# Kernel tuning notes

Measured on AMD Instinct MI355X. Metric: run time of the kernel, lower is better.

The kernel has to match this reference:

```python
import jax, jax.numpy as jnp
import numpy as np

B, Q, G = 32, 16384, 128   # batch, num queries, (padded) num GT per image
K = 32                      # first top-k (nearest candidates per GT)
N = 9                       # second top-k (highest-IoU matches per GT)


def box_cxcywh_to_xyxy(b):
    cx, cy, w, h = jnp.split(b, 4, axis=-1)
    return jnp.concatenate([cx - 0.5 * w, cy - 0.5 * h,
                            cx + 0.5 * w, cy + 0.5 * h], axis=-1)


def box_iou(a, b):
    # a, b: broadcastable [..., 4] in xyxy
    lt = jnp.maximum(a[..., :2], b[..., :2])
    rb = jnp.minimum(a[..., 2:], b[..., 2:])
    wh = jnp.clip(rb - lt, 0.0)
    inter = wh[..., 0] * wh[..., 1]
    area_a = (a[..., 2] - a[..., 0]) * (a[..., 3] - a[..., 1])
    area_b = (b[..., 2] - b[..., 0]) * (b[..., 3] - b[..., 1])
    return inter / (area_a + area_b - inter)


def _assign(gt, pred):
    # gt: [G,4] cxcywh, pred: [Q,4] cxcywh
    # euclidean cdist in cxcywh space: [G, Q]
    d = jnp.sqrt(jnp.sum((gt[:, None, :] - pred[None, :, :]) ** 2, axis=-1))
    # k nearest predictions per GT (smallest distance)
    _, kidx = jax.lax.top_k(-d, K)            # [G, K]
    k_boxes = pred[kidx]                       # [G, K, 4]
    iou = box_iou(box_cxcywh_to_xyxy(gt)[:, None, :],
                  box_cxcywh_to_xyxy(k_boxes))           # [G, K]
    vals, ns = jax.lax.top_k(iou, N)           # [G, N] highest IoU among the K
    pred_idx = jnp.take_along_axis(kidx, ns, axis=1)      # [G, N] global pred ids
    gt_idx = jnp.broadcast_to(jnp.arange(gt.shape[0])[:, None], ns.shape)
    return pred_idx.reshape(-1), gt_idx.reshape(-1)


def setup_inputs() -> dict:
    key = jax.random.key(0)
    k1, k2 = jax.random.split(key)
    pred_boxes = jax.random.uniform(k1, (B, Q, 4), dtype=jnp.float32)
    gt_boxes = jax.random.uniform(k2, (B, G, 4), dtype=jnp.float32)
    return {"pred_boxes": pred_boxes, "gt_boxes": gt_boxes}


def reference(pred_boxes, gt_boxes):
    # per-image assignment, vectorized over the batch
    pred_idx, gt_idx = jax.vmap(_assign)(gt_boxes, pred_boxes)
    # pred_idx, gt_idx: [B, G*N] int32 (analog of the list of (i, j) index tensors)
    return pred_idx, gt_idx
```

## Files before the change

### kernel.cpp

```cpp
#include <hip/hip_runtime.h>

#define BB 32
#define QQ 16384
#define GG 128
#define KK 32
#define NN 9
#define TT 16
#define TH 1024
#define RR (QQ / TH)
#define NW (TH / 64)
#define CAP 192
#define ACAP 96
#define UF 4

typedef unsigned long long u64;
typedef unsigned int u32;

#define INFF __uint_as_float(0x7F800000u)

__device__ __forceinline__ u64 pack_asc(float key, u32 idx) {
  return (((u64)__float_as_uint(key)) << 32) | (u64)idx;
}

__device__ __forceinline__ float dist2_ref(const float4 g, const float4 p) {
#pragma clang fp contract(off)
  float dx = g.x - p.x;
  float dy = g.y - p.y;
  float dz = g.z - p.z;
  float dw = g.w - p.w;
  float s = dx * dx + dy * dy;
  s = s + dz * dz;
  s = s + dw * dw;
  return s;
}

__device__ __forceinline__ float iou_ref(const float4 g, const float4 p) {
#pragma clang fp contract(off)
  float gx1 = g.x - 0.5f * g.z, gy1 = g.y - 0.5f * g.w;
  float gx2 = g.x + 0.5f * g.z, gy2 = g.y + 0.5f * g.w;
  float px1 = p.x - 0.5f * p.z, py1 = p.y - 0.5f * p.w;
  float px2 = p.x + 0.5f * p.z, py2 = p.y + 0.5f * p.w;
  float ltx = fmaxf(gx1, px1), lty = fmaxf(gy1, py1);
  float rbx = fminf(gx2, px2), rby = fminf(gy2, py2);
  float wx = fmaxf(rbx - ltx, 0.0f), wy = fmaxf(rby - lty, 0.0f);
  float inter = wx * wy;
  float aa = (gx2 - gx1) * (gy2 - gy1);
  float ab = (px2 - px1) * (py2 - py1);
  return inter / ((aa + ab) - inter);
}

__device__ __forceinline__ u64 bitonic64(u64 v, int lane) {
#pragma unroll
  for (int k = 2; k <= 64; k <<= 1) {
#pragma unroll
    for (int j = k >> 1; j > 0; j >>= 1) {
      u64 o = __shfl_xor(v, j, 64);
      bool up = ((lane & k) == 0);
      bool lower = ((lane & j) == 0);
      v = (lower == up) ? (v < o ? v : o) : (v > o ? v : o);
    }
  }
  return v;
}

__device__ __forceinline__ u64 bitonic32(u64 v, int lane) {
#pragma unroll
  for (int k = 2; k <= 32; k <<= 1) {
#pragma unroll
    for (int j = k >> 1; j > 0; j >>= 1) {
      u64 o = __shfl_xor(v, j, 64);
      bool up = ((lane & k) == 0);
      bool lower = ((lane & j) == 0);
      v = (lower == up) ? (v < o ? v : o) : (v > o ? v : o);
    }
  }
  return v;
}

__device__ __forceinline__ u32 f2ord(float f) {
  u32 b = __float_as_uint(f);
  return (b & 0x80000000u) ? ~b : (b | 0x80000000u);
}
__device__ __forceinline__ float ord2f(u32 k) {
  return __uint_as_float((k & 0x80000000u) ? (k & 0x7FFFFFFFu) : ~k);
}

__global__ __launch_bounds__(TH, 4) void atss_kernel(
    const float4* __restrict__ pred, const float4* __restrict__ gtb,
    int* __restrict__ out) {
  __shared__ float smin[TT][TH];
  __shared__ float ckey[TT][CAP];
  __shared__ unsigned short cidx[TT][CAP];
  __shared__ unsigned short sact[TT][ACAP];
  __shared__ int kidx[TT][KK];
  __shared__ int nC[TT];
  __shared__ int nAct[TT];

  const int t = threadIdx.x;
  const int f = blockIdx.x;
  const int b = (f & 7) * 4 + (f >> 6);
  const int g0 = ((f >> 3) & 7) * TT;

  if (t < TT) {
    nC[t] = 0;
    nAct[t] = 0;
  }

  float4 G[TT];
#pragma unroll
  for (int gg = 0; gg < TT; ++gg) G[gg] = gtb[b * GG + g0 + gg];

  const float4* pb = pred + (size_t)b * QQ;

  float mn[TT];
#pragma unroll
  for (int gg = 0; gg < TT; ++gg) mn[gg] = INFF;

  float4 P[UF];
#pragma unroll
  for (int u = 0; u < UF; ++u) P[u] = pb[t + u * TH];
#pragma unroll
  for (int j = 0; j < RR; j += UF) {
    float4 C[UF];
#pragma unroll
    for (int u = 0; u < UF; ++u) C[u] = P[u];
    if (j + UF < RR) {
#pragma unroll
      for (int u = 0; u < UF; ++u) P[u] = pb[t + (j + UF + u) * TH];
    }
#pragma unroll
    for (int u = 0; u < UF; ++u) {
      float4 p = C[u];
      float pp = fmaf(p.x, p.x, fmaf(p.y, p.y, fmaf(p.z, p.z, p.w * p.w)));
      float qx = p.x + p.x, qy = p.y + p.y, qz = p.z + p.z, qw = p.w + p.w;
#pragma unroll
      for (int gg = 0; gg < TT; ++gg) {
        float acc = fmaf(-G[gg].x, qx, pp);
        acc = fmaf(-G[gg].y, qy, acc);
        acc = fmaf(-G[gg].z, qz, acc);
        acc = fmaf(-G[gg].w, qw, acc);
        mn[gg] = fminf(mn[gg], acc);
      }
    }
  }
#pragma unroll
  for (int gg = 0; gg < TT; ++gg) smin[gg][t] = mn[gg];

  __syncthreads();

  const int w = t >> 6;
  const int lane = t & 63;

  const float4 gt = gtb[b * GG + g0 + w];

  float V[NW];
#pragma unroll
  for (int k = 0; k < NW; ++k) V[k] = smin[w][lane + 64 * k];

  float m1 = INFF, m2 = INFF;
#pragma unroll
  for (int k = 0; k < NW; ++k) {
    float v = V[k];
    float nm1 = fminf(m1, v);
    m2 = fminf(m2, fmaxf(m1, v));
    m1 = nm1;
  }

  u32 k1 = f2ord(m1), k2 = f2ord(m2);
  u32 pref = 0;
#pragma unroll
  for (int bit = 31; bit >= 0; --bit) {
    u32 tr = pref | (1u << bit);
    int c = __popcll(__ballot(k1 < tr)) + __popcll(__ballot(k2 < tr));
    if (c < 32) pref = tr;
  }
  float Us = ord2f(pref);

  float gg2 = fmaf(gt.x, gt.x,
              fmaf(gt.y, gt.y, fmaf(gt.z, gt.z, gt.w * gt.w)));
  const float sUs = Us + fabsf(Us) * 2e-5f + 4e-6f;
  const float T = fmaxf(Us + gg2, 0.0f) * 1.00002f + 4e-6f;

#pragma unroll
  for (int k = 0; k < NW; ++k) {
    if (V[k] <= sUs) {
      int pos = atomicAdd(&nAct[w], 1);
      if (pos < ACAP) sact[w][pos] = (unsigned short)(lane + 64 * k);
    }
  }
  int na = nAct[w];

  if (na <= ACAP) {
    int total = na * RR;
    int it = lane;
    int i0 = 0;
    float4 p0;
    if (it < total) {
      int r = sact[w][it >> 4];
      i0 = r + (it & 15) * TH;
      p0 = pb[i0];
    }
    while (it < total) {
      int itn = it + 64;
      int i1 = 0;
      float4 p1;
      if (itn < total) {
        int r = sact[w][itn >> 4];
        i1 = r + (itn & 15) * TH;
        p1 = pb[i1];
      }
      float d2 = dist2_ref(gt, p0);
      if (d2 <= T) {
        int pos = atomicAdd(&nC[w], 1);
        if (pos < CAP) {
          ckey[w][pos] = d2;
          cidx[w][pos] = (unsigned short)i0;
        }
      }
      it = itn;
      i0 = i1;
      p0 = p1;
    }
  } else {
    for (int r = lane; r < TH; r += 64) {
      for (int j = 0; j < RR; ++j) {
        int i = r + j * TH;
        float d2 = dist2_ref(gt, pb[i]);
        if (d2 <= T) {
          int pos = atomicAdd(&nC[w], 1);
          if (pos < CAP) {
            ckey[w][pos] = d2;
            cidx[w][pos] = (unsigned short)i;
          }
        }
      }
    }
  }
  int n = nC[w];

  if (n > CAP) {
    if (lane == 0) {
      u64 best[KK];
      for (int l = 0; l < KK; ++l) best[l] = ~0ull;
      for (int i = 0; i < QQ; ++i) {
        float d = sqrtf(dist2_ref(gt, pb[i]));
        u64 pk = pack_asc(d, (u32)i);
        if (pk < best[KK - 1]) {
          int pos = KK - 1;
          while (pos > 0 && best[pos - 1] > pk) {
            best[pos] = best[pos - 1];
            --pos;
          }
          best[pos] = pk;
        }
      }
      for (int l = 0; l < KK; ++l) kidx[w][l] = (int)(best[l] & 0xFFFFFFFFull);
    }
  } else if (n <= 64) {
    u64 v = (lane < n) ? pack_asc(sqrtf(ckey[w][lane]), (u32)cidx[w][lane])
                       : ~0ull;
    u64 s = bitonic64(v, lane);
    if (lane < KK) kidx[w][lane] = (int)(s & 0xFFFFFFFFull);
  } else {
    volatile float* vk = ckey[w];
    for (int sel = 0; sel < KK; ++sel) {
      u64 lm = ~0ull;
      int ls = -1;
      for (int s = lane; s < n; s += 64) {
        float d = sqrtf(vk[s]);
        u64 pk = pack_asc(d, (u32)cidx[w][s]);
        if (pk < lm) {
          lm = pk;
          ls = s;
        }
      }
      u64 ww = lm;
#pragma unroll
      for (int j = 32; j > 0; j >>= 1) {
        u64 o = __shfl_xor(ww, j, 64);
        ww = o < ww ? o : ww;
      }
      if (lm == ww && ls >= 0) {
        vk[ls] = INFF;
        kidx[w][sel] = (int)(ww & 0xFFFFFFFFull);
      }
    }
  }

  {
    u64 v = ~0ull;
    if (lane < KK) {
      float iou = iou_ref(gt, pb[kidx[w][lane]]);
      v = (((u64)(~__float_as_uint(iou))) << 32) | (u64)lane;
    }
    u64 s = bitonic32(v, lane);
    if (lane < NN) {
      int pos = (int)(s & 0xFFFFFFFFull);
      int base = (b * GG + g0 + w) * NN + lane;
      out[base] = kidx[w][pos];
      out[BB * GG * NN + base] = g0 + w;
    }
  }
}

extern "C" void kernel_launch(void* const* d_in, const int* in_sizes, int n_in,
                              void* d_out, int out_size, void* d_ws, size_t ws_size,
                              hipStream_t stream) {
  (void)in_sizes;
  (void)n_in;
  (void)out_size;
  (void)d_ws;
  (void)ws_size;
  const float4* pred = (const float4*)d_in[0];
  const float4* gt = (const float4*)d_in[1];
  int* out = (int*)d_out;
  atss_kernel<<<(GG / TT) * BB, TH, 0, stream>>>(pred, gt, out);
}
```

Baseline: 79.47 us.

## Replace shared atomics with ballot compaction and bitonic sorts with rank-based selection

Shared-memory atomic counters for active rows and candidates are replaced by wave-ballot prefix compaction, which removes the LDS atomics and the counter initialisation. The candidate gather loop is restructured with a 4-deep manual prefetch in place of 1-deep. The bitonic sorts for the top-32 distances and top-9 IoU are replaced by O(n) shuffle-based rank counting with ds_permute scatter, which trades log-depth compare-swap stages for a linear shuffle loop.

```diff
diff --git a/kernel.cpp b/kernel.cpp
--- a/kernel.cpp
+++ b/kernel.cpp
@@ -49,34 +49,6 @@
   return inter / ((aa + ab) - inter);
 }
 
-__device__ __forceinline__ u64 bitonic64(u64 v, int lane) {
-#pragma unroll
-  for (int k = 2; k <= 64; k <<= 1) {
-#pragma unroll
-    for (int j = k >> 1; j > 0; j >>= 1) {
-      u64 o = __shfl_xor(v, j, 64);
-      bool up = ((lane & k) == 0);
-      bool lower = ((lane & j) == 0);
-      v = (lower == up) ? (v < o ? v : o) : (v > o ? v : o);
-    }
-  }
-  return v;
-}
-
-__device__ __forceinline__ u64 bitonic32(u64 v, int lane) {
-#pragma unroll
-  for (int k = 2; k <= 32; k <<= 1) {
-#pragma unroll
-    for (int j = k >> 1; j > 0; j >>= 1) {
-      u64 o = __shfl_xor(v, j, 64);
-      bool up = ((lane & k) == 0);
-      bool lower = ((lane & j) == 0);
-      v = (lower == up) ? (v < o ? v : o) : (v > o ? v : o);
-    }
-  }
-  return v;
-}
-
 __device__ __forceinline__ u32 f2ord(float f) {
   u32 b = __float_as_uint(f);
   return (b & 0x80000000u) ? ~b : (b | 0x80000000u);
@@ -93,18 +65,11 @@
   __shared__ unsigned short cidx[TT][CAP];
   __shared__ unsigned short sact[TT][ACAP];
   __shared__ int kidx[TT][KK];
-  __shared__ int nC[TT];
-  __shared__ int nAct[TT];
 
   const int t = threadIdx.x;
   const int f = blockIdx.x;
   const int b = (f & 7) * 4 + (f >> 6);
   const int g0 = ((f >> 3) & 7) * TT;
-
-  if (t < TT) {
-    nC[t] = 0;
-    nAct[t] = 0;
-  }
 
   float4 G[TT];
 #pragma unroll
@@ -150,6 +115,7 @@
 
   const int w = t >> 6;
   const int lane = t & 63;
+  const u64 below = (lane == 0) ? 0ull : ((1ull << lane) - 1ull);
 
   const float4 gt = gtb[b * GG + g0 + w];
 
@@ -181,64 +147,133 @@
   const float sUs = Us + fabsf(Us) * 2e-5f + 4e-6f;
   const float T = fmaxf(Us + gg2, 0.0f) * 1.00002f + 4e-6f;
 
+  int na = 0;
 #pragma unroll
   for (int k = 0; k < NW; ++k) {
-    if (V[k] <= sUs) {
-      int pos = atomicAdd(&nAct[w], 1);
+    bool c = V[k] <= sUs;
+    u64 mask = __ballot(c);
+    if (c) {
+      int pos = na + __popcll(mask & below);
       if (pos < ACAP) sact[w][pos] = (unsigned short)(lane + 64 * k);
     }
-  }
-  int na = nAct[w];
-
+    na += __popcll(mask);
+  }
+
+  int nCand = 0;
   if (na <= ACAP) {
-    int total = na * RR;
-    int it = lane;
-    int i0 = 0;
-    float4 p0;
-    if (it < total) {
-      int r = sact[w][it >> 4];
-      i0 = r + (it & 15) * TH;
-      p0 = pb[i0];
-    }
-    while (it < total) {
-      int itn = it + 64;
-      int i1 = 0;
-      float4 p1;
-      if (itn < total) {
-        int r = sact[w][itn >> 4];
-        i1 = r + (itn & 15) * TH;
-        p1 = pb[i1];
-      }
-      float d2 = dist2_ref(gt, p0);
-      if (d2 <= T) {
-        int pos = atomicAdd(&nC[w], 1);
-        if (pos < CAP) {
-          ckey[w][pos] = d2;
-          cidx[w][pos] = (unsigned short)i0;
-        }
-      }
-      it = itn;
-      i0 = i1;
-      p0 = p1;
-    }
+    const int eo = (lane & 15) * TH;
+    const int e0 = lane >> 4;
+    const int trips = (na + 15) >> 4;
+
+#define ISSUE(ENT, VV, II, PP)                        \
+  {                                                   \
+    int ent_ = (ENT);                                 \
+    VV = ent_ < na;                                   \
+    int ecl_ = VV ? ent_ : 0;                         \
+    II = (int)sact[w][ecl_] + eo;                     \
+    PP = pb[II];                                      \
+  }
+#define PROCESS(VV, II, PP)                           \
+  {                                                   \
+    float d2_ = dist2_ref(gt, PP);                    \
+    bool acc_ = VV && (d2_ <= T);                     \
+    u64 mask_ = __ballot(acc_);                       \
+    if (acc_) {                                       \
+      int pos_ = nCand + __popcll(mask_ & below);     \
+      if (pos_ < CAP) {                               \
+        ckey[w][pos_] = d2_;                          \
+        cidx[w][pos_] = (unsigned short)II;           \
+      }                                               \
+    }                                                 \
+    nCand += __popcll(mask_);                         \
+  }
+
+    bool va, vb, vc, vd;
+    int ia, ib, ic, id;
+    float4 pa, pbx, pc, pd;
+    ISSUE(e0, va, ia, pa);
+    ISSUE(e0 + 4, vb, ib, pbx);
+    ISSUE(e0 + 8, vc, ic, pc);
+    ISSUE(e0 + 12, vd, id, pd);
+    for (int tr = 0; tr < trips; ++tr) {
+      int en = e0 + 16 * (tr + 1);
+      bool nva, nvb, nvc, nvd;
+      int nia, nib, nic, nid;
+      float4 npa, npb, npc, npd;
+      ISSUE(en, nva, nia, npa);
+      ISSUE(en + 4, nvb, nib, npb);
+      ISSUE(en + 8, nvc, nic, npc);
+      ISSUE(en + 12, nvd, nid, npd);
+      PROCESS(va, ia, pa);
+      PROCESS(vb, ib, pbx);
+      PROCESS(vc, ic, pc);
+      PROCESS(vd, id, pd);
+      va = nva; ia = nia; pa = npa;
+      vb = nvb; ib = nib; pbx = npb;
+      vc = nvc; ic = nic; pc = npc;
+      vd = nvd; id = nid; pd = npd;
+    }
+#undef ISSUE
+#undef PROCESS
   } else {
-    for (int r = lane; r < TH; r += 64) {
+    for (int rr = 0; rr < NW; ++rr) {
+      int r = lane + 64 * rr;
       for (int j = 0; j < RR; ++j) {
         int i = r + j * TH;
         float d2 = dist2_ref(gt, pb[i]);
-        if (d2 <= T) {
-          int pos = atomicAdd(&nC[w], 1);
+        bool acc = d2 <= T;
+        u64 mask = __ballot(acc);
+        if (acc) {
+          int pos = nCand + __popcll(mask & below);
           if (pos < CAP) {
             ckey[w][pos] = d2;
             cidx[w][pos] = (unsigned short)i;
           }
         }
-      }
-    }
-  }
-  int n = nC[w];
-
-  if (n > CAP) {
+        nCand += __popcll(mask);
+      }
+    }
+  }
+  const int n = nCand;
+
+  int selIdx = 0;
+  if (n <= 64) {
+    bool valid = lane < n;
+    float myd = valid ? sqrtf(ckey[w][lane]) : 0.0f;
+    u32 myi = valid ? (u32)cidx[w][lane] : 0u;
+    u64 mk = valid ? pack_asc(myd, myi) : ~0ull;
+    int rank = 0;
+    for (int i = 0; i < n; ++i) {
+      u64 ki = __shfl(mk, i, 64);
+      rank += (ki < mk) ? 1 : 0;
+    }
+    selIdx = __builtin_amdgcn_ds_permute(rank << 2, (int)myi);
+  } else if (n <= CAP) {
+    volatile float* vk = ckey[w];
+    for (int sel = 0; sel < KK; ++sel) {
+      u64 lm = ~0ull;
+      int ls = -1;
+      for (int s = lane; s < n; s += 64) {
+        float d = sqrtf(vk[s]);
+        u64 pk = pack_asc(d, (u32)cidx[w][s]);
+        if (pk < lm) {
+          lm = pk;
+          ls = s;
+        }
+      }
+      u64 ww = lm;
+#pragma unroll
+      for (int j = 32; j > 0; j >>= 1) {
+        u64 o = __shfl_xor(ww, j, 64);
+        ww = o < ww ? o : ww;
+      }
+      if (lm == ww && ls >= 0) {
+        vk[ls] = INFF;
+        kidx[w][sel] = (int)(ww & 0xFFFFFFFFull);
+      }
+    }
+    selIdx = kidx[w][lane & 31];
+  } else {
     if (lane == 0) {
       u64 best[KK];
       for (int l = 0; l < KK; ++l) best[l] = ~0ull;
@@ -256,48 +291,25 @@
       }
       for (int l = 0; l < KK; ++l) kidx[w][l] = (int)(best[l] & 0xFFFFFFFFull);
     }
-  } else if (n <= 64) {
-    u64 v = (lane < n) ? pack_asc(sqrtf(ckey[w][lane]), (u32)cidx[w][lane])
-                       : ~0ull;
-    u64 s = bitonic64(v, lane);
-    if (lane < KK) kidx[w][lane] = (int)(s & 0xFFFFFFFFull);
-  } else {
-    volatile float* vk = ckey[w];
-    for (int sel = 0; sel < KK; ++sel) {
-      u64 lm = ~0ull;
-      int ls = -1;
-      for (int s = lane; s < n; s += 64) {
-        float d = sqrtf(vk[s]);
-        u64 pk = pack_asc(d, (u32)cidx[w][s]);
-        if (pk < lm) {
-          lm = pk;
-          ls = s;
-        }
-      }
-      u64 ww = lm;
-#pragma unroll
-      for (int j = 32; j > 0; j >>= 1) {
-        u64 o = __shfl_xor(ww, j, 64);
-        ww = o < ww ? o : ww;
-      }
-      if (lm == ww && ls >= 0) {
-        vk[ls] = INFF;
-        kidx[w][sel] = (int)(ww & 0xFFFFFFFFull);
-      }
-    }
+    selIdx = kidx[w][lane & 31];
   }
 
   {
-    u64 v = ~0ull;
+    float iou = 0.0f;
+    u32 pi = 0;
     if (lane < KK) {
-      float iou = iou_ref(gt, pb[kidx[w][lane]]);
-      v = (((u64)(~__float_as_uint(iou))) << 32) | (u64)lane;
-    }
-    u64 s = bitonic32(v, lane);
-    if (lane < NN) {
-      int pos = (int)(s & 0xFFFFFFFFull);
-      int base = (b * GG + g0 + w) * NN + lane;
-      out[base] = kidx[w][pos];
+      pi = (u32)selIdx;
+      iou = iou_ref(gt, pb[pi]);
+    }
+    u32 ik = (lane < KK) ? ~__float_as_uint(iou) : 0xFFFFFFFFu;
+    int r9 = 0;
+    for (int i = 0; i < KK; ++i) {
+      u32 ki = __shfl(ik, i, 64);
+      r9 += ((ki < ik) || (ki == ik && i < lane)) ? 1 : 0;
+    }
+    if (lane < KK && r9 < NN) {
+      int base = (b * GG + g0 + w) * NN + r9;
+      out[base] = (int)pi;
       out[BB * GG * NN + base] = g0 + w;
     }
   }
```

New measurement: 81.40 us. 2.4% more time.
